# Kernel optimization log

Hardware: AMD Instinct MI355X
Metric: run time of the kernel (lower is better)

Reference implementation:

```python
import jax, jax.numpy as jnp
import numpy as np

B, T, V, F = 8, 12, 2048, 16
K_CHEB, C = 3, 64

def setup_inputs() -> dict:
    key = jax.random.key(0)
    k1, k2, k3, k4 = jax.random.split(key, 4)
    x = jax.random.normal(k1, (B, T, V, F), dtype=jnp.float32)
    Att = jax.random.uniform(k2, (B, V, V), dtype=jnp.float32)
    cheb = jax.random.normal(k3, (K_CHEB, V, V), dtype=jnp.float32) / np.sqrt(V)
    theta = jax.random.normal(k4, (K_CHEB, F, C), dtype=jnp.float32) * 0.05
    return {"x": x, "Att": Att, "cheb": cheb, "theta": theta}

def reference(x, Att, cheb, theta):
    # Attention-masked Chebyshev polynomials: S_k[b,u,v] = T_k[u,v] * Att[b,u,v]
    # (dropout from the original training-time call is omitted: eval mode)
    masked = cheb[:, None, :, :] * Att[None, :, :, :]            # (K,B,V,V)
    # rhs[b,v,f] = sum_u S_k[b,u,v] * x[b,t,u,f]  (transpose+batch_dot)
    rhs = jnp.einsum('kbuv,btuf->kbtvf', masked, x)              # (K,B,T,V,F)
    # sum over Chebyshev order k of rhs @ Theta_k, then relu
    out = jnp.einsum('kbtvf,kfc->btvc', rhs, theta)              # (B,T,V,C)
    return jax.nn.relu(out)
```

## Files before the change

### kernel.cpp

```cpp
#include <hip/hip_runtime.h>
#include <hip/hip_bf16.h>
#include <stdint.h>

#define B_  8
#define T_  12
#define V_  2048
#define F_  16
#define K_  3
#define C_  64
#define N_  192

typedef _Float16 f16;
typedef _Float16 half4v __attribute__((ext_vector_type(4)));
typedef _Float16 half8v __attribute__((ext_vector_type(8)));
typedef float    f32x4  __attribute__((ext_vector_type(4)));
typedef float    f32x16 __attribute__((ext_vector_type(16)));
typedef unsigned int u32;

__global__ __launch_bounds__(256) void prep_xt(const float* __restrict__ x,
                                               f16* __restrict__ XT) {
  int bid = blockIdx.x;
  int bt = bid >> 2, uc = bid & 3;
  int b = bt / T_, t = bt % T_;
  __shared__ float tile[64][17];
  int r  = threadIdx.x >> 2, fq = threadIdx.x & 3;
  int f  = threadIdx.x >> 4, uq = threadIdx.x & 15;
  for (int u0 = uc * 512; u0 < uc * 512 + 512; u0 += 64) {
    f32x4 v = *(const f32x4*)(x + ((size_t)(b * T_ + t) * V_ + u0 + r) * F_ + fq * 4);
    tile[r][fq * 4 + 0] = v[0];
    tile[r][fq * 4 + 1] = v[1];
    tile[r][fq * 4 + 2] = v[2];
    tile[r][fq * 4 + 3] = v[3];
    __syncthreads();
    half4v h;
    h[0] = (f16)tile[uq * 4 + 0][f];
    h[1] = (f16)tile[uq * 4 + 1][f];
    h[2] = (f16)tile[uq * 4 + 2][f];
    h[3] = (f16)tile[uq * 4 + 3][f];
    *(half4v*)(XT + (size_t)(b * N_ + t * F_ + f) * V_ + u0 + uq * 4) = h;
    __syncthreads();
  }
}

template<int UH>
__global__ __launch_bounds__(256, 2) void gemm_fused(const float* __restrict__ Att,
                                                     const float* __restrict__ cheb,
                                                     const f16* __restrict__ XT,
                                                     f16* __restrict__ rhs) {
  constexpr int NSTEP = (V_ / UH) / 64;
  const int bid = blockIdx.x;
  const int b  = bid / (32 * UH);
  const int rr = bid % (32 * UH);
  const int vt = rr / UH, uh = rr % UH;
  const int vbase = vt * 64;
  const size_t ubase = (size_t)uh * (V_ / UH);

  __shared__ char smem[49152];
  char* Ab = smem;
  char* Bb = smem + 24576;

  const int tid = threadIdx.x;
  const int wave = tid >> 6, lane = tid & 63;
  const int wm = wave >> 1, wn = wave & 1;
  const int vsub = (tid & 15) * 4, usub = (tid >> 4) * 4;

  const float* attb  = Att + (size_t)b * V_ * V_ + vbase + vsub + (size_t)usub * V_;
  const float* chebb = cheb + vbase + vsub + (size_t)usub * V_;
  const f16*   xtb   = XT + (size_t)b * N_ * V_;

  f32x16 acc[3][3];
#pragma unroll
  for (int k = 0; k < 3; ++k)
#pragma unroll
    for (int nf = 0; nf < 3; ++nf) acc[k][nf] = 0;

  const int vrow = wm * 32 + (lane & 31);
  const int akey = ((vrow >> 2) & 7) << 4;
  int nrowA[3], bkeyA[3];
#pragma unroll
  for (int nf = 0; nf < 3; ++nf) {
    nrowA[nf] = wn * 96 + nf * 32 + (lane & 31);
    bkeyA[nf] = (nrowA[nf] & 7) << 4;
  }
  const int wkey = (tid & 7) << 4;
  const int gl_c = (lane & 7) ^ (lane >> 3);

  auto stageB = [&](size_t u) {
#pragma unroll
    for (int e = 0; e < 6; ++e) {
      int slot = wave * 6 + e;
      int n = slot * 8 + (lane >> 3);
      const f16* src = xtb + (size_t)n * V_ + u + gl_c * 8;
      __builtin_amdgcn_global_load_lds((const __attribute__((address_space(1))) u32*)src,
                                       (__attribute__((address_space(3))) u32*)(Bb + slot * 1024),
                                       16, 0, 0);
    }
  };
  auto writeA = [&](half4v pk[3][4]) {
#pragma unroll
    for (int k = 0; k < 3; ++k)
#pragma unroll
      for (int j = 0; j < 4; ++j)
        *(half4v*)(Ab + k * 8192 + (vsub + j) * 128 + ((usub * 2) ^ wkey)) = pk[k][j];
  };

  {
    f32x4 pa[4], cv[3][4];
#pragma unroll
    for (int i = 0; i < 4; ++i) pa[i] = *(const f32x4*)(attb + (ubase + i) * V_);
#pragma unroll
    for (int k = 0; k < 3; ++k)
#pragma unroll
      for (int i = 0; i < 4; ++i)
        cv[k][i] = *(const f32x4*)(chebb + (size_t)k * V_ * V_ + (ubase + i) * V_);
    stageB(ubase);
    half4v pk[3][4];
#pragma unroll
    for (int k = 0; k < 3; ++k)
#pragma unroll
      for (int j = 0; j < 4; ++j) {
        half4v h;
        h[0] = (f16)(cv[k][0][j] * pa[0][j]); h[1] = (f16)(cv[k][1][j] * pa[1][j]);
        h[2] = (f16)(cv[k][2][j] * pa[2][j]); h[3] = (f16)(cv[k][3][j] * pa[3][j]);
        pk[k][j] = h;
      }
    writeA(pk);
    __syncthreads();
  }

#define COMPUTE_KS(ks)                                                          \
  {                                                                             \
    const int ku2 = (ks) * 32 + (lane >> 5) * 16;                               \
    half8v bfr0 = *(const half8v*)(Bb + nrowA[0] * 128 + (ku2 ^ bkeyA[0]));     \
    half8v bfr1 = *(const half8v*)(Bb + nrowA[1] * 128 + (ku2 ^ bkeyA[1]));     \
    half8v bfr2 = *(const half8v*)(Bb + nrowA[2] * 128 + (ku2 ^ bkeyA[2]));     \
    __builtin_amdgcn_s_setprio(1);                                              \
    _Pragma("unroll")                                                           \
    for (int k = 0; k < 3; ++k) {                                               \
      half8v a = *(const half8v*)(Ab + k * 8192 + vrow * 128 + (ku2 ^ akey));   \
      acc[k][0] = __builtin_amdgcn_mfma_f32_32x32x16_f16(a, bfr0, acc[k][0], 0, 0, 0); \
      acc[k][1] = __builtin_amdgcn_mfma_f32_32x32x16_f16(a, bfr1, acc[k][1], 0, 0, 0); \
      acc[k][2] = __builtin_amdgcn_mfma_f32_32x32x16_f16(a, bfr2, acc[k][2], 0, 0, 0); \
    }                                                                           \
    __builtin_amdgcn_s_setprio(0);                                              \
  }

  for (int t = 0; t < NSTEP; ++t) {
    const bool pref = (t + 1) < NSTEP;
    const size_t unext = ubase + (size_t)(t + 1) * 64;
    f32x4 pa[4], cv[3][4];
    half4v pk[3][4];

    if (pref) {
#pragma unroll
      for (int i = 0; i < 4; ++i) pa[i] = *(const f32x4*)(attb + (unext + i) * V_);
#pragma unroll
      for (int k = 0; k < 3; ++k)
#pragma unroll
        for (int i = 0; i < 4; ++i)
          cv[k][i] = *(const f32x4*)(chebb + (size_t)k * V_ * V_ + (unext + i) * V_);
    }

    COMPUTE_KS(0)
    COMPUTE_KS(1)

    if (pref) {
#pragma unroll
      for (int k = 0; k < 3; ++k)
#pragma unroll
        for (int j = 0; j < 4; ++j) {
          half4v h;
          h[0] = (f16)(cv[k][0][j] * pa[0][j]); h[1] = (f16)(cv[k][1][j] * pa[1][j]);
          h[2] = (f16)(cv[k][2][j] * pa[2][j]); h[3] = (f16)(cv[k][3][j] * pa[3][j]);
          pk[k][j] = h;
        }
    }

    COMPUTE_KS(2)
    COMPUTE_KS(3)

    __syncthreads();
    if (pref) {
      stageB(unext);
      writeA(pk);
      __syncthreads();
    }
  }
#undef COMPUTE_KS

#pragma unroll
  for (int nf = 0; nf < 3; ++nf) {
    int n = wn * 96 + nf * 32 + (lane & 31);
    int tt = n >> 4, fi = n & 15;
#pragma unroll
    for (int k = 0; k < 3; ++k) {
#pragma unroll
      for (int r = 0; r < 16; ++r) {
        int v = vbase + wm * 32 + (r & 3) + 8 * (r >> 2) + 4 * (lane >> 5);
        rhs[((size_t)(b * T_ + tt) * V_ + v) * (48 * UH) + uh * 48 + k * 16 + fi] =
            (f16)acc[k][nf][r];
      }
    }
  }
}

template<int UH>
__global__ __launch_bounds__(256) void epi(const f16* __restrict__ rhs,
                                           const float* __restrict__ theta,
                                           float* __restrict__ out) {
  int wave = threadIdx.x >> 6, lane = threadIdx.x & 63;
  int row0 = blockIdx.x * 128 + wave * 32;
  int cl = lane & 31, kh = (lane >> 5) * 8;

  half8v bf[2][3];
#pragma unroll
  for (int nf = 0; nf < 2; ++nf)
#pragma unroll
    for (int ks = 0; ks < 3; ++ks) {
      half8v hb;
#pragma unroll
      for (int j = 0; j < 8; ++j)
        hb[j] = (f16)theta[(size_t)(ks * 16 + kh + j) * C_ + nf * 32 + cl];
      bf[nf][ks] = hb;
    }

  f32x16 acc0 = 0, acc1 = 0;
#pragma unroll
  for (int s = 0; s < 3 * UH; ++s) {
    half8v a = *(const half8v*)(rhs + (size_t)(row0 + cl) * (48 * UH) + s * 16 + kh);
    acc0 = __builtin_amdgcn_mfma_f32_32x32x16_f16(a, bf[0][s % 3], acc0, 0, 0, 0);
    acc1 = __builtin_amdgcn_mfma_f32_32x32x16_f16(a, bf[1][s % 3], acc1, 0, 0, 0);
  }
#pragma unroll
  for (int r = 0; r < 16; ++r) {
    int row = row0 + (r & 3) + 8 * (r >> 2) + 4 * (lane >> 5);
    out[(size_t)row * C_ + cl]      = fmaxf(acc0[r], 0.f);
    out[(size_t)row * C_ + 32 + cl] = fmaxf(acc1[r], 0.f);
  }
}

extern "C" void kernel_launch(void* const* d_in, const int* in_sizes, int n_in,
                              void* d_out, int out_size, void* d_ws, size_t ws_size,
                              hipStream_t stream) {
  const float* x     = (const float*)d_in[0];
  const float* Att   = (const float*)d_in[1];
  const float* cheb  = (const float*)d_in[2];
  const float* theta = (const float*)d_in[3];
  float* out = (float*)d_out;

  const size_t xtB   = (size_t)B_ * N_ * V_ * sizeof(f16);
  const size_t rhsB2 = (size_t)B_ * T_ * V_ * 96 * sizeof(f16);

  f16* XT  = (f16*)d_ws;
  f16* rhs = (f16*)((char*)d_ws + xtB);

  prep_xt<<<B_ * T_ * 4, 256, 0, stream>>>(x, XT);
  if (ws_size >= xtB + rhsB2) {
    gemm_fused<2><<<B_ * 32 * 2, 256, 0, stream>>>(Att, cheb, XT, rhs);
    epi<2><<<(B_ * T_ * V_) / 128, 256, 0, stream>>>(rhs, theta, out);
  } else {
    gemm_fused<1><<<B_ * 32, 256, 0, stream>>>(Att, cheb, XT, rhs);
    epi<1><<<(B_ * T_ * V_) / 128, 256, 0, stream>>>(rhs, theta, out);
  }
}
```

Measured before the change: 107.2 us.

## Pre-convert cheb to fp16, double-buffer XT staging, batch-interleave block order

Adds a prep kernel that converts the Chebyshev matrices to fp16 once per call, so the main GEMM streams half the bytes for cheb and forms the masked product in fp16. The XT tile staging now uses two LDS buffers, so the next tile's async load is issued before the current MFMA steps instead of after the barrier. Block indexing is reordered so consecutive blocks take different batches and can share cheb tiles in cache. The cost is an extra kernel pass over cheb, more LDS per block (possible occupancy loss), and slightly lower precision from the fp16 multiply.

```diff
diff --git a/kernel.cpp b/kernel.cpp
--- a/kernel.cpp
+++ b/kernel.cpp
@@ -42,98 +42,21 @@
   }
 }
 
-template<int UH>
-__global__ __launch_bounds__(256, 2) void gemm_fused(const float* __restrict__ Att,
-                                                     const float* __restrict__ cheb,
-                                                     const f16* __restrict__ XT,
-                                                     f16* __restrict__ rhs) {
-  constexpr int NSTEP = (V_ / UH) / 64;
-  const int bid = blockIdx.x;
-  const int b  = bid / (32 * UH);
-  const int rr = bid % (32 * UH);
-  const int vt = rr / UH, uh = rr % UH;
-  const int vbase = vt * 64;
-  const size_t ubase = (size_t)uh * (V_ / UH);
-
-  __shared__ char smem[49152];
-  char* Ab = smem;
-  char* Bb = smem + 24576;
-
-  const int tid = threadIdx.x;
-  const int wave = tid >> 6, lane = tid & 63;
-  const int wm = wave >> 1, wn = wave & 1;
-  const int vsub = (tid & 15) * 4, usub = (tid >> 4) * 4;
-
-  const float* attb  = Att + (size_t)b * V_ * V_ + vbase + vsub + (size_t)usub * V_;
-  const float* chebb = cheb + vbase + vsub + (size_t)usub * V_;
-  const f16*   xtb   = XT + (size_t)b * N_ * V_;
-
-  f32x16 acc[3][3];
-#pragma unroll
-  for (int k = 0; k < 3; ++k)
-#pragma unroll
-    for (int nf = 0; nf < 3; ++nf) acc[k][nf] = 0;
-
-  const int vrow = wm * 32 + (lane & 31);
-  const int akey = ((vrow >> 2) & 7) << 4;
-  int nrowA[3], bkeyA[3];
-#pragma unroll
-  for (int nf = 0; nf < 3; ++nf) {
-    nrowA[nf] = wn * 96 + nf * 32 + (lane & 31);
-    bkeyA[nf] = (nrowA[nf] & 7) << 4;
-  }
-  const int wkey = (tid & 7) << 4;
-  const int gl_c = (lane & 7) ^ (lane >> 3);
-
-  auto stageB = [&](size_t u) {
-#pragma unroll
-    for (int e = 0; e < 6; ++e) {
-      int slot = wave * 6 + e;
-      int n = slot * 8 + (lane >> 3);
-      const f16* src = xtb + (size_t)n * V_ + u + gl_c * 8;
-      __builtin_amdgcn_global_load_lds((const __attribute__((address_space(1))) u32*)src,
-                                       (__attribute__((address_space(3))) u32*)(Bb + slot * 1024),
-                                       16, 0, 0);
-    }
-  };
-  auto writeA = [&](half4v pk[3][4]) {
-#pragma unroll
-    for (int k = 0; k < 3; ++k)
-#pragma unroll
-      for (int j = 0; j < 4; ++j)
-        *(half4v*)(Ab + k * 8192 + (vsub + j) * 128 + ((usub * 2) ^ wkey)) = pk[k][j];
-  };
-
-  {
-    f32x4 pa[4], cv[3][4];
-#pragma unroll
-    for (int i = 0; i < 4; ++i) pa[i] = *(const f32x4*)(attb + (ubase + i) * V_);
-#pragma unroll
-    for (int k = 0; k < 3; ++k)
-#pragma unroll
-      for (int i = 0; i < 4; ++i)
-        cv[k][i] = *(const f32x4*)(chebb + (size_t)k * V_ * V_ + (ubase + i) * V_);
-    stageB(ubase);
-    half4v pk[3][4];
-#pragma unroll
-    for (int k = 0; k < 3; ++k)
-#pragma unroll
-      for (int j = 0; j < 4; ++j) {
-        half4v h;
-        h[0] = (f16)(cv[k][0][j] * pa[0][j]); h[1] = (f16)(cv[k][1][j] * pa[1][j]);
-        h[2] = (f16)(cv[k][2][j] * pa[2][j]); h[3] = (f16)(cv[k][3][j] * pa[3][j]);
-        pk[k][j] = h;
-      }
-    writeA(pk);
-    __syncthreads();
-  }
-
-#define COMPUTE_KS(ks)                                                          \
+__global__ __launch_bounds__(256) void prep_cheb(const float* __restrict__ c,
+                                                 f16* __restrict__ c16) {
+  size_t i = ((size_t)blockIdx.x * 256 + threadIdx.x) * 4;
+  f32x4 v = *(const f32x4*)(c + i);
+  half4v h;
+  h[0] = (f16)v[0]; h[1] = (f16)v[1]; h[2] = (f16)v[2]; h[3] = (f16)v[3];
+  *(half4v*)(c16 + i) = h;
+}
+
+#define COMPUTE_KS(ks, BPTR)                                                    \
   {                                                                             \
     const int ku2 = (ks) * 32 + (lane >> 5) * 16;                               \
-    half8v bfr0 = *(const half8v*)(Bb + nrowA[0] * 128 + (ku2 ^ bkeyA[0]));     \
-    half8v bfr1 = *(const half8v*)(Bb + nrowA[1] * 128 + (ku2 ^ bkeyA[1]));     \
-    half8v bfr2 = *(const half8v*)(Bb + nrowA[2] * 128 + (ku2 ^ bkeyA[2]));     \
+    half8v bfr0 = *(const half8v*)((BPTR) + nrowA[0] * 128 + (ku2 ^ bkeyA[0])); \
+    half8v bfr1 = *(const half8v*)((BPTR) + nrowA[1] * 128 + (ku2 ^ bkeyA[1])); \
+    half8v bfr2 = *(const half8v*)((BPTR) + nrowA[2] * 128 + (ku2 ^ bkeyA[2])); \
     __builtin_amdgcn_s_setprio(1);                                              \
     _Pragma("unroll")                                                           \
     for (int k = 0; k < 3; ++k) {                                               \
@@ -145,48 +68,151 @@
     __builtin_amdgcn_s_setprio(0);                                              \
   }
 
+template<int UH, bool F16C>
+__global__ __launch_bounds__(256, 2) void gemm_fused(const float* __restrict__ Att,
+                                                     const void* __restrict__ chebp,
+                                                     const f16* __restrict__ XT,
+                                                     f16* __restrict__ rhs) {
+  constexpr int NSTEP = (V_ / UH) / 64;
+  const int bid = blockIdx.x;
+  const int b  = bid & 7;
+  const int r2 = bid >> 3;
+  const int vt = r2 / UH, uh = r2 % UH;
+  const int vbase = vt * 64;
+  const size_t ubase = (size_t)uh * (V_ / UH);
+
+  __shared__ char smem[73728];
+  char* Ab = smem;
+  char* Bbuf0 = smem + 24576;
+  char* Bbuf1 = smem + 49152;
+
+  const int tid = threadIdx.x;
+  const int wave = tid >> 6, lane = tid & 63;
+  const int wm = wave >> 1, wn = wave & 1;
+  const int vsub = (tid & 15) * 4, usub = (tid >> 4) * 4;
+
+  const float* attb   = Att + (size_t)b * V_ * V_ + vbase + vsub + (size_t)usub * V_;
+  const f16*   cb16   = (const f16*)chebp + vbase + vsub + (size_t)usub * V_;
+  const float* cbf    = (const float*)chebp + vbase + vsub + (size_t)usub * V_;
+  const f16*   xtb    = XT + (size_t)b * N_ * V_;
+
+  f32x16 acc[3][3];
+#pragma unroll
+  for (int k = 0; k < 3; ++k)
+#pragma unroll
+    for (int nf = 0; nf < 3; ++nf) acc[k][nf] = 0;
+
+  const int vrow = wm * 32 + (lane & 31);
+  const int akey = ((vrow >> 2) & 7) << 4;
+  int nrowA[3], bkeyA[3];
+#pragma unroll
+  for (int nf = 0; nf < 3; ++nf) {
+    nrowA[nf] = wn * 96 + nf * 32 + (lane & 31);
+    bkeyA[nf] = (nrowA[nf] & 7) << 4;
+  }
+  const int wkey = (tid & 7) << 4;
+  const int gl_c = (lane & 7) ^ (lane >> 3);
+
+  f32x4  pa[4];
+  half4v cv16[3][4];
+  f32x4  cvf[3][4];
+
+  auto stageB = [&](size_t u, char* Bb) {
+#pragma unroll
+    for (int e = 0; e < 6; ++e) {
+      int slot = wave * 6 + e;
+      int n = slot * 8 + (lane >> 3);
+      const f16* src = xtb + (size_t)n * V_ + u + gl_c * 8;
+      __builtin_amdgcn_global_load_lds((const __attribute__((address_space(1))) u32*)src,
+                                       (__attribute__((address_space(3))) u32*)(Bb + slot * 1024),
+                                       16, 0, 0);
+    }
+  };
+  auto issueA = [&](size_t u) {
+#pragma unroll
+    for (int i = 0; i < 4; ++i) pa[i] = *(const f32x4*)(attb + (u + i) * V_);
+    if constexpr (F16C) {
+#pragma unroll
+      for (int k = 0; k < 3; ++k)
+#pragma unroll
+        for (int i = 0; i < 4; ++i)
+          cv16[k][i] = *(const half4v*)(cb16 + (size_t)k * V_ * V_ + (u + i) * V_);
+    } else {
+#pragma unroll
+      for (int k = 0; k < 3; ++k)
+#pragma unroll
+        for (int i = 0; i < 4; ++i)
+          cvf[k][i] = *(const f32x4*)(cbf + (size_t)k * V_ * V_ + (u + i) * V_);
+    }
+  };
+  auto makePk = [&](half4v pk[3][4]) {
+    if constexpr (F16C) {
+      half4v a16[4];
+#pragma unroll
+      for (int i = 0; i < 4; ++i) {
+        a16[i][0] = (f16)pa[i][0]; a16[i][1] = (f16)pa[i][1];
+        a16[i][2] = (f16)pa[i][2]; a16[i][3] = (f16)pa[i][3];
+      }
+#pragma unroll
+      for (int k = 0; k < 3; ++k)
+#pragma unroll
+        for (int j = 0; j < 4; ++j) {
+          half4v h;
+          h[0] = cv16[k][0][j] * a16[0][j]; h[1] = cv16[k][1][j] * a16[1][j];
+          h[2] = cv16[k][2][j] * a16[2][j]; h[3] = cv16[k][3][j] * a16[3][j];
+          pk[k][j] = h;
+        }
+    } else {
+#pragma unroll
+      for (int k = 0; k < 3; ++k)
+#pragma unroll
+        for (int j = 0; j < 4; ++j) {
+          half4v h;
+          h[0] = (f16)(cvf[k][0][j] * pa[0][j]); h[1] = (f16)(cvf[k][1][j] * pa[1][j]);
+          h[2] = (f16)(cvf[k][2][j] * pa[2][j]); h[3] = (f16)(cvf[k][3][j] * pa[3][j]);
+          pk[k][j] = h;
+        }
+    }
+  };
+  auto writeA = [&](half4v pk[3][4]) {
+#pragma unroll
+    for (int k = 0; k < 3; ++k)
+#pragma unroll
+      for (int j = 0; j < 4; ++j)
+        *(half4v*)(Ab + k * 8192 + (vsub + j) * 128 + ((usub * 2) ^ wkey)) = pk[k][j];
+  };
+
+  issueA(ubase);
+  stageB(ubase, Bbuf0);
+  {
+    half4v pk[3][4];
+    makePk(pk);
+    writeA(pk);
+  }
+  __syncthreads();
+
   for (int t = 0; t < NSTEP; ++t) {
+    char* Bc = (t & 1) ? Bbuf1 : Bbuf0;
+    char* Bn = (t & 1) ? Bbuf0 : Bbuf1;
     const bool pref = (t + 1) < NSTEP;
     const size_t unext = ubase + (size_t)(t + 1) * 64;
-    f32x4 pa[4], cv[3][4];
+
+    if (pref) {
+      issueA(unext);
+      stageB(unext, Bn);
+    }
+
+    COMPUTE_KS(0, Bc)
+    COMPUTE_KS(1, Bc)
+    COMPUTE_KS(2, Bc)
+    COMPUTE_KS(3, Bc)
+
     half4v pk[3][4];
-
-    if (pref) {
-#pragma unroll
-      for (int i = 0; i < 4; ++i) pa[i] = *(const f32x4*)(attb + (unext + i) * V_);
-#pragma unroll
-      for (int k = 0; k < 3; ++k)
-#pragma unroll
-        for (int i = 0; i < 4; ++i)
-          cv[k][i] = *(const f32x4*)(chebb + (size_t)k * V_ * V_ + (unext + i) * V_);
-    }
-
-    COMPUTE_KS(0)
-    COMPUTE_KS(1)
-
-    if (pref) {
-#pragma unroll
-      for (int k = 0; k < 3; ++k)
-#pragma unroll
-        for (int j = 0; j < 4; ++j) {
-          half4v h;
-          h[0] = (f16)(cv[k][0][j] * pa[0][j]); h[1] = (f16)(cv[k][1][j] * pa[1][j]);
-          h[2] = (f16)(cv[k][2][j] * pa[2][j]); h[3] = (f16)(cv[k][3][j] * pa[3][j]);
-          pk[k][j] = h;
-        }
-    }
-
-    COMPUTE_KS(2)
-    COMPUTE_KS(3)
-
+    if (pref) makePk(pk);
     __syncthreads();
-    if (pref) {
-      stageB(unext);
-      writeA(pk);
-      __syncthreads();
-    }
-  }
-#undef COMPUTE_KS
+    if (pref) writeA(pk);
+    __syncthreads();
+  }
 
 #pragma unroll
   for (int nf = 0; nf < 3; ++nf) {
@@ -203,6 +229,7 @@
     }
   }
 }
+#undef COMPUTE_KS
 
 template<int UH>
 __global__ __launch_bounds__(256) void epi(const f16* __restrict__ rhs,
@@ -249,17 +276,28 @@
   float* out = (float*)d_out;
 
   const size_t xtB   = (size_t)B_ * N_ * V_ * sizeof(f16);
-  const size_t rhsB2 = (size_t)B_ * T_ * V_ * 96 * sizeof(f16);
-
-  f16* XT  = (f16*)d_ws;
-  f16* rhs = (f16*)((char*)d_ws + xtB);
-
+  const size_t rhs2B = (size_t)B_ * T_ * V_ * 96 * sizeof(f16);
+  const size_t rhs1B = rhs2B / 2;
+  const size_t chB   = (size_t)K_ * V_ * V_ * sizeof(f16);
+
+  f16* XT = (f16*)d_ws;
   prep_xt<<<B_ * T_ * 4, 256, 0, stream>>>(x, XT);
-  if (ws_size >= xtB + rhsB2) {
-    gemm_fused<2><<<B_ * 32 * 2, 256, 0, stream>>>(Att, cheb, XT, rhs);
+
+  if (ws_size >= xtB + rhs2B + chB) {
+    f16* rhs = (f16*)((char*)d_ws + xtB);
+    f16* c16 = (f16*)((char*)d_ws + xtB + rhs2B);
+    prep_cheb<<<(K_ * V_ * V_) / 1024, 256, 0, stream>>>(cheb, c16);
+    gemm_fused<2, true><<<B_ * 32 * 2, 256, 0, stream>>>(Att, c16, XT, rhs);
     epi<2><<<(B_ * T_ * V_) / 128, 256, 0, stream>>>(rhs, theta, out);
+  } else if (ws_size >= xtB + rhs1B + chB) {
+    f16* rhs = (f16*)((char*)d_ws + xtB);
+    f16* c16 = (f16*)((char*)d_ws + xtB + rhs1B);
+    prep_cheb<<<(K_ * V_ * V_) / 1024, 256, 0, stream>>>(cheb, c16);
+    gemm_fused<1, true><<<B_ * 32, 256, 0, stream>>>(Att, c16, XT, rhs);
+    epi<1><<<(B_ * T_ * V_) / 128, 256, 0, stream>>>(rhs, theta, out);
   } else {
-    gemm_fused<1><<<B_ * 32, 256, 0, stream>>>(Att, cheb, XT, rhs);
+    f16* rhs = (f16*)((char*)d_ws + xtB);
+    gemm_fused<1, false><<<B_ * 32, 256, 0, stream>>>(Att, cheb, XT, rhs);
     epi<1><<<(B_ * T_ * V_) / 128, 256, 0, stream>>>(rhs, theta, out);
   }
 }
```

Result: slower. 118.0 us (+10.1%).
